# Performance work log

Hardware: AMD Instinct MI355X
Metric: run time of the kernel (lower is better)

The kernel has to match this reference:

```python
import jax, jax.numpy as jnp
import numpy as np

N_NODES = 100000
N_EDGES = 3200000
N_GRAPHS = 1024
K = 32  # total number of kernels (num_kernel1..4 = 8 each)


def setup_inputs() -> dict:
    key = jax.random.key(0)
    ks = jax.random.split(key, 20)
    inp = {
        'x': jax.random.normal(ks[0], (N_NODES, 5), jnp.float32),
        'p': jax.random.normal(ks[1], (N_NODES, 3), jnp.float32),
        'edge_attr': jax.random.normal(ks[2], (N_EDGES, 1), jnp.float32),
        'Wx0': jax.random.normal(ks[3], (5, K), jnp.float32) * 0.3,
        'Wx1': jax.random.normal(ks[4], (K, K), jnp.float32) * 0.1,
        'Wx2': jax.random.normal(ks[5], (K, K), jnp.float32) * 0.1,
        'Wp0': jax.random.normal(ks[6], (3, K), jnp.float32) * 0.3,
        'Wp1': jax.random.normal(ks[7], (3, K), jnp.float32) * 0.3,
        'Wp2': jax.random.normal(ks[8], (3, K), jnp.float32) * 0.3,
        'We0': jax.random.normal(ks[9], (1, K), jnp.float32) * 0.3,
        'We1': jax.random.normal(ks[10], (1, K), jnp.float32) * 0.3,
        'We2': jax.random.normal(ks[11], (1, K), jnp.float32) * 0.3,
        'b0': jax.random.normal(ks[12], (K,), jnp.float32) * 0.1,
        'b1': jax.random.normal(ks[13], (K,), jnp.float32) * 0.1,
        'b2': jax.random.normal(ks[14], (K,), jnp.float32) * 0.1,
        'Wh': jax.random.normal(ks[15], (K, 1), jnp.float32) * 0.1,
        'bh': jax.random.normal(ks[16], (1,), jnp.float32) * 0.1,
        'edge_index': jax.random.randint(ks[17], (2, N_EDGES), 0, N_NODES, jnp.int64 if jax.config.jax_enable_x64 else jnp.int32),
        'batch': jnp.sort(jax.random.randint(ks[18], (N_NODES,), 0, N_GRAPHS, jnp.int64 if jax.config.jax_enable_x64 else jnp.int32)),
    }
    return inp


def _gnn_forward(x, p, edge_attr, Wxs, Wps, Wes, bs, edge_index):
    src, dst = edge_index[0], edge_index[1]
    p_rel = p[src] - p[dst]                      # [E, 3] relative positions
    h = x
    for Wx, Wp, We, b in zip(Wxs, Wps, Wes, bs):
        # kernel similarity per edge: gather neighbor feats + geometry, score vs K kernels
        msg = jnp.tanh(h[src] @ Wx + p_rel @ Wp + edge_attr @ We + b)   # [E, K]
        sim_sc = jax.ops.segment_sum(msg, dst, num_segments=N_NODES)    # [N, K] node sim scores
        # MolGCN.propagate: message(sim_sc_j) with aggr='add'
        h = jax.ops.segment_sum(sim_sc[src], dst, num_segments=N_NODES)  # [N, K]
    return h


def reference(x, p, edge_attr, Wx0, Wx1, Wx2, Wp0, Wp1, Wp2, We0, We1, We2,
              b0, b1, b2, Wh, bh, edge_index, batch):
    h = _gnn_forward(x, p, edge_attr, (Wx0, Wx1, Wx2), (Wp0, Wp1, Wp2),
                     (We0, We1, We2), (b0, b1, b2), edge_index)
    # global_mean_pool over graphs
    sums = jax.ops.segment_sum(h, batch, num_segments=N_GRAPHS)          # [G, K]
    cnt = jax.ops.segment_sum(jnp.ones((N_NODES,), h.dtype), batch, num_segments=N_GRAPHS)
    graph_rep = sums / jnp.maximum(cnt, 1.0)[:, None]                    # [G, K]
    pred = graph_rep @ Wh + bh                                           # [G, 1]
    return (pred, graph_rep)
```

## Files before the change

### kernel.cpp

```cpp
#include <hip/hip_runtime.h>
#include <hip/hip_fp16.h>

#define K_DIM 32
#define BN 256
#define MAXBUCK 512
#define CAP 10240
#define TANH_SCALE 2.8853900817779268f

typedef float f32x2 __attribute__((ext_vector_type(2)));

__device__ __forceinline__ void pk_add(f32x2& acc, f32x2 v) {
    asm("v_pk_add_f32 %0, %1, %0" : "+v"(acc) : "v"(v));
}


__global__ void k_bcnt(const int* __restrict__ dst, int* __restrict__ bcnt,
                       int E, int nbuck) {
    __shared__ int h[MAXBUCK];
    for (int i = threadIdx.x; i < nbuck; i += blockDim.x) h[i] = 0;
    __syncthreads();
    for (int e = blockIdx.x * blockDim.x + threadIdx.x; e < E; e += gridDim.x * blockDim.x)
        atomicAdd(&h[dst[e] >> 8], 1);
    __syncthreads();
    for (int i = threadIdx.x; i < nbuck; i += blockDim.x)
        if (h[i]) atomicAdd(&bcnt[i], h[i]);
}

__global__ void k_bscan(const int* __restrict__ bcnt, int* __restrict__ boff,
                        int* __restrict__ gcur, int nbuck, int total) {
    __shared__ int sm[256];
    __shared__ int carry;
    int t = threadIdx.x;
    if (t == 0) carry = 0;
    __syncthreads();
    for (int base = 0; base < nbuck; base += 256) {
        int v = (base + t < nbuck) ? bcnt[base + t] : 0;
        sm[t] = v;
        __syncthreads();
        #pragma unroll
        for (int d = 1; d < 256; d <<= 1) {
            int tv = (t >= d) ? sm[t - d] : 0;
            __syncthreads();
            sm[t] += tv;
            __syncthreads();
        }
        int excl = carry + sm[t] - v;
        if (base + t < nbuck) { boff[base + t] = excl; gcur[base + t] = excl; }
        __syncthreads();
        if (t == 0) carry += sm[255];
        __syncthreads();
    }
    if (t == 0) boff[nbuck] = total;
}

__global__ void k_bscatter(const int* __restrict__ src, const int* __restrict__ dst,
                           const float* __restrict__ ea, int* __restrict__ gcur,
                           uint2* __restrict__ rec, int E, int nbuck) {
    __shared__ int lcnt[MAXBUCK];
    __shared__ int lbase[MAXBUCK];
    const int nb = gridDim.x;
    const long c0 = (long)E * blockIdx.x / nb;
    const long c1 = (long)E * (blockIdx.x + 1) / nb;
    for (int i = threadIdx.x; i < nbuck; i += blockDim.x) lcnt[i] = 0;
    __syncthreads();
    for (long e = c0 + threadIdx.x; e < c1; e += blockDim.x)
        atomicAdd(&lcnt[dst[e] >> 8], 1);
    __syncthreads();
    for (int i = threadIdx.x; i < nbuck; i += blockDim.x) {
        int c = lcnt[i];
        lbase[i] = c ? atomicAdd(&gcur[i], c) : 0;
    }
    __syncthreads();
    for (int i = threadIdx.x; i < nbuck; i += blockDim.x) lcnt[i] = 0;
    __syncthreads();
    for (long e = c0 + threadIdx.x; e < c1; e += blockDim.x) {
        int d = dst[e];
        int b = d >> 8;
        int rank = atomicAdd(&lcnt[b], 1);
        unsigned meta = ((unsigned)(d & 255) << 17) | (unsigned)src[e];
        rec[lbase[b] + rank] = make_uint2(meta, __float_as_uint(ea[e]));
    }
}

__global__ void k_blocal(const uint2* __restrict__ rec, uint2* __restrict__ rec2,
                         int* __restrict__ srcs2, const int* __restrict__ boff,
                         int* __restrict__ off, int N, int E) {
    __shared__ uint2 sB[CAP];
    __shared__ int cnt[BN];
    __shared__ int base[BN];
    __shared__ int sm[BN];
    const int b = blockIdx.x;
    const int tid = threadIdx.x;
    int e0 = boff[b], e1 = boff[b + 1];
    int tot = e1 - e0;
    cnt[tid] = 0;
    __syncthreads();
    for (int i = tid; i < tot; i += 256)
        atomicAdd(&cnt[rec[e0 + i].x >> 17], 1);
    __syncthreads();
    int v = cnt[tid];
    sm[tid] = v;
    __syncthreads();
    #pragma unroll
    for (int d = 1; d < 256; d <<= 1) {
        int tv = (tid >= d) ? sm[tid - d] : 0;
        __syncthreads();
        sm[tid] += tv;
        __syncthreads();
    }
    base[tid] = sm[tid] - v;
    int n = b * BN + tid;
    if (n < N) off[n] = e0 + base[tid];
    if (b == 0 && tid == 0) off[N] = E;
    cnt[tid] = 0;
    __syncthreads();
    for (int i = tid; i < tot; i += 256) {
        uint2 r = rec[e0 + i];
        int dl = r.x >> 17;
        int rank = atomicAdd(&cnt[dl], 1);
        unsigned s = r.x & 0x1FFFFu;
        float eaf = __uint_as_float(r.y);
        unsigned hb = (unsigned)__half_as_ushort(__float2half(eaf));
        sB[base[dl] + rank] = make_uint2(s, (hb << 16) | hb);
    }
    __syncthreads();
    for (int i = tid; i < tot; i += 256) {
        uint2 r = sB[i];
        rec2[e0 + i] = r;
        srcs2[e0 + i] = (int)r.x;
    }
}

__global__ void k_initdummy(__half* __restrict__ Mh, __half* __restrict__ simh, int N) {
    int i = threadIdx.x;
    Mh[N * 32 + i] = __ushort_as_half((unsigned short)0x7C00);
    simh[N * 32 + i] = __ushort_as_half((unsigned short)0);
}


__global__ void k_node_gemm5(const float* __restrict__ h, const float* __restrict__ p,
                             const float* __restrict__ Wx, const float* __restrict__ Wp,
                             __half* __restrict__ Mh, int n_nodes) {
    __shared__ float sWx[5 * 32];
    __shared__ float sWp[96];
    for (int i = threadIdx.x; i < 5 * 32; i += blockDim.x) sWx[i] = Wx[i] * TANH_SCALE;
    if (threadIdx.x < 96) sWp[threadIdx.x] = Wp[threadIdx.x] * TANH_SCALE;
    __syncthreads();
    const int k = threadIdx.x & 31;
    int n = blockIdx.x * (blockDim.x >> 5) + (threadIdx.x >> 5);
    if (n >= n_nodes) return;
    float hv = (k < 5) ? h[n * 5 + k] : 0.0f;
    float pv = (k < 3) ? p[n * 3 + k] : 0.0f;
    float acc = 0.0f;
    #pragma unroll
    for (int j = 0; j < 5; ++j) acc = fmaf(__shfl(hv, j, 32), sWx[j * 32 + k], acc);
    #pragma unroll
    for (int j = 0; j < 3; ++j) acc = fmaf(__shfl(pv, j, 32), sWp[j * 32 + k], acc);
    Mh[n * 32 + k] = __float2half(acc);
}

__global__ void k_edge_msg(const __half* __restrict__ Mh, const float* __restrict__ p,
                           const int* __restrict__ off, const uint2* __restrict__ rec,
                           const float* __restrict__ Wp, const float* __restrict__ We,
                           const float* __restrict__ bias,
                           __half* __restrict__ simh, int N) {
    __shared__ uint2 stage[8][32];
    const int l = threadIdx.x & 31;
    const int c = l & 15;
    const int q = l >> 4;
    const int grp = threadIdx.x >> 5;
    int n = blockIdx.x * 8 + grp;
    if (n >= N) return;

    const __half2* Mh2 = (const __half2*)Mh;

    float2 wef = ((const float2*)We)[c];
    __half2 we2 = __floats2half2_rn(wef.x * TANH_SCALE, wef.y * TANH_SCALE);
    float2 b2  = ((const float2*)bias)[c];
    float2 wp0 = ((const float2*)Wp)[c];
    float2 wp1 = ((const float2*)(Wp + 32))[c];
    float2 wp2 = ((const float2*)(Wp + 64))[c];
    float pn = (l < 3) ? p[n * 3 + l] : 0.0f;
    float pn0 = __shfl(pn, 0, 32), pn1 = __shfl(pn, 1, 32), pn2 = __shfl(pn, 2, 32);
    __half2 cnst2 = __floats2half2_rn(
        (b2.x - (pn0 * wp0.x + pn1 * wp1.x + pn2 * wp2.x)) * TANH_SCALE,
        (b2.y - (pn0 * wp0.y + pn1 * wp1.y + pn2 * wp2.y)) * TANH_SCALE);
    const __half2 one2  = __floats2half2_rn(1.0f, 1.0f);
    const __half2 zero2 = __floats2half2_rn(0.0f, 0.0f);

    float fx = 0.0f, fy = 0.0f;
    int e0 = off[n], e1 = off[n + 1];
    for (int base = e0; base < e1; base += 32) {
        int m = min(32, e1 - base);
        uint2 r = (l < m) ? rec[base + l] : make_uint2((unsigned)N, 0u);
        stage[grp][l] = r;
        __half2 acc2 = zero2;
        for (int j = 0; j < m; j += 16) {
            __half2 mv[8], av[8];
            #pragma unroll
            for (int u = 0; u < 8; ++u) {
                uint2 e = stage[grp][j + 2 * u + q];
                unsigned eb = e.y;
                av[u] = *(const __half2*)&eb;
                mv[u] = Mh2[e.x * 16 + c];
            }
            #pragma unroll
            for (int u = 0; u < 8; ++u) {
                __half2 arg = __hadd2(__hfma2(av[u], we2, cnst2), mv[u]);
                __half2 ex  = h2exp2(arg);
                __half2 rr  = h2rcp(__hadd2(ex, one2));
                acc2 = __hadd2(acc2, rr);
            }
        }
        fx += __low2float(acc2);
        fy += __high2float(acc2);
    }
    fx += __shfl_xor(fx, 16, 32);
    fy += __shfl_xor(fy, 16, 32);
    float deg = (float)(e1 - e0);
    if (l < 16)
        ((__half2*)simh)[n * 16 + c] =
            __floats2half2_rn(fmaf(-2.0f, fx, deg), fmaf(-2.0f, fy, deg));
}

template <int FUSE>
__global__ void k_prop_gemm(const __half* __restrict__ simh, const int* __restrict__ off,
                            const int* __restrict__ srcs, const float* __restrict__ p,
                            const float* __restrict__ Wx, const float* __restrict__ Wp,
                            __half* __restrict__ outMh, float* __restrict__ outF,
                            int N) {
    __shared__ float sWx[1024];
    __shared__ int stageS[8][32];
    if (FUSE) {
        for (int i = threadIdx.x; i < 1024; i += blockDim.x) sWx[i] = Wx[i] * TANH_SCALE;
        __syncthreads();
    }
    const int l = threadIdx.x & 31;
    const int c = l & 15;
    const int q = l >> 4;
    const int grp = threadIdx.x >> 5;
    int n = blockIdx.x * 8 + grp;
    if (n >= N) return;

    const __half2* sim2 = (const __half2*)simh;
    f32x2 facc = {0.0f, 0.0f};
    int e0 = off[n], e1 = off[n + 1];
    for (int base = e0; base < e1; base += 32) {
        int m = min(32, e1 - base);
        stageS[grp][l] = (l < m) ? srcs[base + l] : N;
        for (int j = 0; j < m; j += 16) {
            __half2 v[8];
            #pragma unroll
            for (int u = 0; u < 8; ++u) {
                int s = stageS[grp][j + 2 * u + q];
                v[u] = sim2[s * 16 + c];
            }
            #pragma unroll
            for (int u = 0; u < 8; ++u) {
                float2 fv = __half22float2(v[u]);
                f32x2 t = {fv.x, fv.y};
                pk_add(facc, t);
            }
        }
    }
    float fx = facc.x, fy = facc.y;
    fx += __shfl_xor(fx, 16, 32);
    fy += __shfl_xor(fy, 16, 32);

    if (!FUSE) {
        if (l < 16) ((float2*)outF)[n * 16 + c] = make_float2(fx, fy);
        return;
    }
    float mm = 0.0f;
    #pragma unroll
    for (int i = 0; i < 16; ++i) {
        float hx = __shfl(fx, i, 32);
        float hy = __shfl(fy, i, 32);
        mm = fmaf(hx, sWx[(2 * i) * 32 + l], mm);
        mm = fmaf(hy, sWx[(2 * i + 1) * 32 + l], mm);
    }
    float pv = (l < 3) ? p[n * 3 + l] : 0.0f;
    float pp = __shfl(pv, 0, 32) * Wp[l] + __shfl(pv, 1, 32) * Wp[32 + l]
             + __shfl(pv, 2, 32) * Wp[64 + l];
    mm = fmaf(pp, TANH_SCALE, mm);
    outMh[n * 32 + l] = __float2half(mm);
}


__global__ void k_pool(const float* __restrict__ h, const int* __restrict__ batch,
                       const float* __restrict__ Wh, const float* __restrict__ bh,
                       float* __restrict__ out, int n_nodes, int n_graphs) {
    __shared__ int sLo, sHi;
    __shared__ float red[256];
    int g = blockIdx.x;
    if (threadIdx.x == 0) {
        int lo = 0, hi = n_nodes;
        while (lo < hi) { int m = (lo + hi) >> 1; if (batch[m] < g) lo = m + 1; else hi = m; }
        sLo = lo;
        lo = 0; hi = n_nodes; int g1 = g + 1;
        while (lo < hi) { int m = (lo + hi) >> 1; if (batch[m] < g1) lo = m + 1; else hi = m; }
        sHi = lo;
    }
    __syncthreads();
    int lo = sLo, hi = sHi;
    int k = threadIdx.x & 31, r = threadIdx.x >> 5;
    float acc = 0.0f;
    for (int n = lo + r; n < hi; n += 8) acc += h[n * 32 + k];
    red[threadIdx.x] = acc;
    __syncthreads();
    if (threadIdx.x < 32) {
        float s = 0.0f;
        #pragma unroll
        for (int r2 = 0; r2 < 8; ++r2) s += red[r2 * 32 + k];
        float c = (float)(hi - lo);
        float rep = s / fmaxf(c, 1.0f);
        out[n_graphs + g * 32 + k] = rep;
        float t = rep * Wh[k];
        #pragma unroll
        for (int d = 16; d > 0; d >>= 1) t += __shfl_down(t, d, 32);
        if (k == 0) out[g] = t + bh[0];
    }
}


extern "C" void kernel_launch(void* const* d_in, const int* in_sizes, int n_in,
                              void* d_out, int out_size, void* d_ws, size_t ws_size,
                              hipStream_t stream) {
    const float* x   = (const float*)d_in[0];
    const float* p   = (const float*)d_in[1];
    const float* ea  = (const float*)d_in[2];
    const float* Wx0 = (const float*)d_in[3];
    const float* Wx1 = (const float*)d_in[4];
    const float* Wx2 = (const float*)d_in[5];
    const float* Wp0 = (const float*)d_in[6];
    const float* Wp1 = (const float*)d_in[7];
    const float* Wp2 = (const float*)d_in[8];
    const float* We0 = (const float*)d_in[9];
    const float* We1 = (const float*)d_in[10];
    const float* We2 = (const float*)d_in[11];
    const float* b0  = (const float*)d_in[12];
    const float* b1  = (const float*)d_in[13];
    const float* b2  = (const float*)d_in[14];
    const float* Wh  = (const float*)d_in[15];
    const float* bh  = (const float*)d_in[16];
    const int* edge_index = (const int*)d_in[17];
    const int* batch      = (const int*)d_in[18];

    const int N = in_sizes[0] / 5;
    const int E = in_sizes[17] / 2;
    const int G = out_size / 33;
    const int nbuck = (N + BN - 1) / BN;

    const int* srcp = edge_index;
    const int* dstp = edge_index + E;

    char* w = (char*)d_ws;
    auto alloc = [&](size_t bytes) -> void* {
        void* r = (void*)w;
        w += (bytes + 255) & ~(size_t)255;
        return r;
    };
    int*    bcnt  = (int*)alloc((size_t)nbuck * 4);
    int*    boff  = (int*)alloc((size_t)(nbuck + 1) * 4);
    int*    gcur  = (int*)alloc((size_t)nbuck * 4);
    int*    off   = (int*)alloc((size_t)(N + 1) * 4);
    uint2*  rec   = (uint2*)alloc((size_t)E * 8);
    uint2*  rec2  = (uint2*)alloc((size_t)E * 8);
    int*    srcs2 = (int*)alloc((size_t)E * 4);
    __half* Mh    = (__half*)alloc((size_t)(N + 1) * K_DIM * 2);
    __half* simh  = (__half*)alloc((size_t)(N + 1) * K_DIM * 2);
    float*  hB    = (float*)alloc((size_t)N * K_DIM * 4);

    (void)hipMemsetAsync(bcnt, 0, (size_t)nbuck * 4, stream);
    k_bcnt<<<1024, 256, 0, stream>>>(dstp, bcnt, E, nbuck);
    k_bscan<<<1, 256, 0, stream>>>(bcnt, boff, gcur, nbuck, E);
    k_bscatter<<<256, 1024, 0, stream>>>(srcp, dstp, ea, gcur, rec, E, nbuck);
    k_blocal<<<nbuck, 256, 0, stream>>>(rec, rec2, srcs2, boff, off, N, E);
    k_initdummy<<<1, 32, 0, stream>>>(Mh, simh, N);

    const int NB = (N + 7) / 8;

    k_node_gemm5<<<NB, 256, 0, stream>>>(x, p, Wx0, Wp0, Mh, N);
    k_edge_msg<<<NB, 256, 0, stream>>>(Mh, p, off, rec2, Wp0, We0, b0, simh, N);
    k_prop_gemm<1><<<NB, 256, 0, stream>>>(simh, off, srcs2, p, Wx1, Wp1, Mh, nullptr, N);
    k_edge_msg<<<NB, 256, 0, stream>>>(Mh, p, off, rec2, Wp1, We1, b1, simh, N);
    k_prop_gemm<1><<<NB, 256, 0, stream>>>(simh, off, srcs2, p, Wx2, Wp2, Mh, nullptr, N);
    k_edge_msg<<<NB, 256, 0, stream>>>(Mh, p, off, rec2, Wp2, We2, b2, simh, N);
    k_prop_gemm<0><<<NB, 256, 0, stream>>>(simh, off, srcs2, p, nullptr, nullptr, nullptr, hB, N);

    k_pool<<<G, 256, 0, stream>>>(hB, batch, Wh, bh, (float*)d_out, N, G);
}
```

Before: 398.3 us.

## Split 32-wide features into two 16-column halves for cache-resident gathers

Node features and similarity scores are stored as two separate 16-column half arrays, and the edge-message and propagation kernels run twice per layer, once per half. Each half-array is about 3.2MB, so the random gathers can stay cache-resident instead of hitting the full 6.4MB table. The node GEMM is moved out of the propagation kernel into a separate 32x32 kernel reading fp32 hF. Edge record and source index loads now use nontemporal hints. The cost is reading the edge lists twice per layer and adding extra kernel launches.

Result: slower. 576.7 us (+44.8%).

```diff
diff --git a/kernel.cpp b/kernel.cpp
--- a/kernel.cpp
+++ b/kernel.cpp
@@ -1,7 +1,6 @@
 #include <hip/hip_runtime.h>
 #include <hip/hip_fp16.h>
 
-#define K_DIM 32
 #define BN 256
 #define MAXBUCK 512
 #define CAP 10240
@@ -131,16 +130,22 @@
     }
 }
 
-__global__ void k_initdummy(__half* __restrict__ Mh, __half* __restrict__ simh, int N) {
+__global__ void k_initdummy(__half* __restrict__ Mh0, __half* __restrict__ Mh1,
+                            __half* __restrict__ s0, __half* __restrict__ s1, int N) {
     int i = threadIdx.x;
-    Mh[N * 32 + i] = __ushort_as_half((unsigned short)0x7C00);
-    simh[N * 32 + i] = __ushort_as_half((unsigned short)0);
+    if (i < 16) {
+        Mh0[N * 16 + i] = __ushort_as_half((unsigned short)0x7C00);
+        Mh1[N * 16 + i] = __ushort_as_half((unsigned short)0x7C00);
+        s0[N * 16 + i] = __ushort_as_half((unsigned short)0);
+        s1[N * 16 + i] = __ushort_as_half((unsigned short)0);
+    }
 }
 
 
 __global__ void k_node_gemm5(const float* __restrict__ h, const float* __restrict__ p,
                              const float* __restrict__ Wx, const float* __restrict__ Wp,
-                             __half* __restrict__ Mh, int n_nodes) {
+                             __half* __restrict__ Mh0, __half* __restrict__ Mh1,
+                             int n_nodes) {
     __shared__ float sWx[5 * 32];
     __shared__ float sWp[96];
     for (int i = threadIdx.x; i < 5 * 32; i += blockDim.x) sWx[i] = Wx[i] * TANH_SCALE;
@@ -156,30 +161,54 @@
     for (int j = 0; j < 5; ++j) acc = fmaf(__shfl(hv, j, 32), sWx[j * 32 + k], acc);
     #pragma unroll
     for (int j = 0; j < 3; ++j) acc = fmaf(__shfl(pv, j, 32), sWp[j * 32 + k], acc);
-    Mh[n * 32 + k] = __float2half(acc);
-}
-
-__global__ void k_edge_msg(const __half* __restrict__ Mh, const float* __restrict__ p,
-                           const int* __restrict__ off, const uint2* __restrict__ rec,
-                           const float* __restrict__ Wp, const float* __restrict__ We,
-                           const float* __restrict__ bias,
-                           __half* __restrict__ simh, int N) {
+    __half hh = __float2half(acc);
+    if (k < 16) Mh0[n * 16 + k] = hh; else Mh1[n * 16 + (k & 15)] = hh;
+}
+
+__global__ void k_node_gemm32(const float* __restrict__ hF, const float* __restrict__ p,
+                              const float* __restrict__ Wx, const float* __restrict__ Wp,
+                              __half* __restrict__ Mh0, __half* __restrict__ Mh1,
+                              int n_nodes) {
+    __shared__ float sWx[1024];
+    __shared__ float sWp[96];
+    for (int i = threadIdx.x; i < 1024; i += blockDim.x) sWx[i] = Wx[i] * TANH_SCALE;
+    if (threadIdx.x < 96) sWp[threadIdx.x] = Wp[threadIdx.x] * TANH_SCALE;
+    __syncthreads();
+    const int k = threadIdx.x & 31;
+    int n = blockIdx.x * (blockDim.x >> 5) + (threadIdx.x >> 5);
+    if (n >= n_nodes) return;
+    float hv = hF[n * 32 + k];
+    float pv = (k < 3) ? p[n * 3 + k] : 0.0f;
+    float acc = 0.0f;
+    #pragma unroll
+    for (int j = 0; j < 32; ++j) acc = fmaf(__shfl(hv, j, 32), sWx[j * 32 + k], acc);
+    #pragma unroll
+    for (int j = 0; j < 3; ++j) acc = fmaf(__shfl(pv, j, 32), sWp[j * 32 + k], acc);
+    __half hh = __float2half(acc);
+    if (k < 16) Mh0[n * 16 + k] = hh; else Mh1[n * 16 + (k & 15)] = hh;
+}
+
+__global__ void k_edge_half(const __half* __restrict__ MhH, const float* __restrict__ p,
+                            const int* __restrict__ off, const uint2* __restrict__ rec,
+                            const float* __restrict__ WpH, const float* __restrict__ WeH,
+                            const float* __restrict__ biasH,
+                            __half* __restrict__ simH, int N) {
     __shared__ uint2 stage[8][32];
     const int l = threadIdx.x & 31;
-    const int c = l & 15;
-    const int q = l >> 4;
+    const int c = l & 7;
+    const int q = l >> 3;
     const int grp = threadIdx.x >> 5;
     int n = blockIdx.x * 8 + grp;
     if (n >= N) return;
 
-    const __half2* Mh2 = (const __half2*)Mh;
-
-    float2 wef = ((const float2*)We)[c];
+    const __half2* MhH2 = (const __half2*)MhH;
+
+    float2 wef = ((const float2*)WeH)[c];
     __half2 we2 = __floats2half2_rn(wef.x * TANH_SCALE, wef.y * TANH_SCALE);
-    float2 b2  = ((const float2*)bias)[c];
-    float2 wp0 = ((const float2*)Wp)[c];
-    float2 wp1 = ((const float2*)(Wp + 32))[c];
-    float2 wp2 = ((const float2*)(Wp + 64))[c];
+    float2 b2  = ((const float2*)biasH)[c];
+    float2 wp0 = ((const float2*)WpH)[c];
+    float2 wp1 = ((const float2*)(WpH + 32))[c];
+    float2 wp2 = ((const float2*)(WpH + 64))[c];
     float pn = (l < 3) ? p[n * 3 + l] : 0.0f;
     float pn0 = __shfl(pn, 0, 32), pn1 = __shfl(pn, 1, 32), pn2 = __shfl(pn, 2, 32);
     __half2 cnst2 = __floats2half2_rn(
@@ -188,102 +217,74 @@
     const __half2 one2  = __floats2half2_rn(1.0f, 1.0f);
     const __half2 zero2 = __floats2half2_rn(0.0f, 0.0f);
 
+    const unsigned long long* rec8 = (const unsigned long long*)rec;
     float fx = 0.0f, fy = 0.0f;
     int e0 = off[n], e1 = off[n + 1];
     for (int base = e0; base < e1; base += 32) {
         int m = min(32, e1 - base);
-        uint2 r = (l < m) ? rec[base + l] : make_uint2((unsigned)N, 0u);
-        stage[grp][l] = r;
+        unsigned long long rv = (l < m) ? __builtin_nontemporal_load(rec8 + base + l)
+                                        : (unsigned long long)(unsigned)N;
+        stage[grp][l] = make_uint2((unsigned)rv, (unsigned)(rv >> 32));
+        __half2 mv[8], av[8];
+        #pragma unroll
+        for (int u = 0; u < 8; ++u) {
+            uint2 e = stage[grp][4 * u + q];
+            unsigned eb = e.y;
+            av[u] = *(const __half2*)&eb;
+            mv[u] = MhH2[e.x * 8 + c];
+        }
         __half2 acc2 = zero2;
-        for (int j = 0; j < m; j += 16) {
-            __half2 mv[8], av[8];
-            #pragma unroll
-            for (int u = 0; u < 8; ++u) {
-                uint2 e = stage[grp][j + 2 * u + q];
-                unsigned eb = e.y;
-                av[u] = *(const __half2*)&eb;
-                mv[u] = Mh2[e.x * 16 + c];
-            }
-            #pragma unroll
-            for (int u = 0; u < 8; ++u) {
-                __half2 arg = __hadd2(__hfma2(av[u], we2, cnst2), mv[u]);
-                __half2 ex  = h2exp2(arg);
-                __half2 rr  = h2rcp(__hadd2(ex, one2));
-                acc2 = __hadd2(acc2, rr);
-            }
+        #pragma unroll
+        for (int u = 0; u < 8; ++u) {
+            __half2 arg = __hadd2(__hfma2(av[u], we2, cnst2), mv[u]);
+            acc2 = __hadd2(acc2, h2rcp(__hadd2(h2exp2(arg), one2)));
         }
         fx += __low2float(acc2);
         fy += __high2float(acc2);
     }
-    fx += __shfl_xor(fx, 16, 32);
-    fy += __shfl_xor(fy, 16, 32);
+    fx += __shfl_xor(fx, 8, 32); fx += __shfl_xor(fx, 16, 32);
+    fy += __shfl_xor(fy, 8, 32); fy += __shfl_xor(fy, 16, 32);
     float deg = (float)(e1 - e0);
-    if (l < 16)
-        ((__half2*)simh)[n * 16 + c] =
+    if (l < 8)
+        ((__half2*)simH)[n * 8 + c] =
             __floats2half2_rn(fmaf(-2.0f, fx, deg), fmaf(-2.0f, fy, deg));
 }
 
-template <int FUSE>
-__global__ void k_prop_gemm(const __half* __restrict__ simh, const int* __restrict__ off,
-                            const int* __restrict__ srcs, const float* __restrict__ p,
-                            const float* __restrict__ Wx, const float* __restrict__ Wp,
-                            __half* __restrict__ outMh, float* __restrict__ outF,
-                            int N) {
-    __shared__ float sWx[1024];
+__global__ void k_prop_half(const __half* __restrict__ simH, const int* __restrict__ off,
+                            const int* __restrict__ srcs, float* __restrict__ hF,
+                            int colbase, int N) {
     __shared__ int stageS[8][32];
-    if (FUSE) {
-        for (int i = threadIdx.x; i < 1024; i += blockDim.x) sWx[i] = Wx[i] * TANH_SCALE;
-        __syncthreads();
-    }
     const int l = threadIdx.x & 31;
-    const int c = l & 15;
-    const int q = l >> 4;
+    const int c = l & 7;
+    const int q = l >> 3;
     const int grp = threadIdx.x >> 5;
     int n = blockIdx.x * 8 + grp;
     if (n >= N) return;
 
-    const __half2* sim2 = (const __half2*)simh;
+    const __half2* sim2 = (const __half2*)simH;
     f32x2 facc = {0.0f, 0.0f};
     int e0 = off[n], e1 = off[n + 1];
     for (int base = e0; base < e1; base += 32) {
         int m = min(32, e1 - base);
-        stageS[grp][l] = (l < m) ? srcs[base + l] : N;
-        for (int j = 0; j < m; j += 16) {
-            __half2 v[8];
-            #pragma unroll
-            for (int u = 0; u < 8; ++u) {
-                int s = stageS[grp][j + 2 * u + q];
-                v[u] = sim2[s * 16 + c];
-            }
-            #pragma unroll
-            for (int u = 0; u < 8; ++u) {
-                float2 fv = __half22float2(v[u]);
-                f32x2 t = {fv.x, fv.y};
-                pk_add(facc, t);
-            }
+        stageS[grp][l] = (l < m) ? __builtin_nontemporal_load(srcs + base + l) : N;
+        __half2 v[8];
+        #pragma unroll
+        for (int u = 0; u < 8; ++u) {
+            int s = stageS[grp][4 * u + q];
+            v[u] = sim2[s * 8 + c];
         }
+        #pragma unroll
+        for (int u = 0; u < 8; ++u) {
+            float2 fv = __half22float2(v[u]);
+            f32x2 t = {fv.x, fv.y};
+            pk_add(facc, t);
+        }
     }
     float fx = facc.x, fy = facc.y;
-    fx += __shfl_xor(fx, 16, 32);
-    fy += __shfl_xor(fy, 16, 32);
-
-    if (!FUSE) {
-        if (l < 16) ((float2*)outF)[n * 16 + c] = make_float2(fx, fy);
-        return;
-    }
-    float mm = 0.0f;
-    #pragma unroll
-    for (int i = 0; i < 16; ++i) {
-        float hx = __shfl(fx, i, 32);
-        float hy = __shfl(fy, i, 32);
-        mm = fmaf(hx, sWx[(2 * i) * 32 + l], mm);
-        mm = fmaf(hy, sWx[(2 * i + 1) * 32 + l], mm);
-    }
-    float pv = (l < 3) ? p[n * 3 + l] : 0.0f;
-    float pp = __shfl(pv, 0, 32) * Wp[l] + __shfl(pv, 1, 32) * Wp[32 + l]
-             + __shfl(pv, 2, 32) * Wp[64 + l];
-    mm = fmaf(pp, TANH_SCALE, mm);
-    outMh[n * 32 + l] = __float2half(mm);
+    fx += __shfl_xor(fx, 8, 32); fx += __shfl_xor(fx, 16, 32);
+    fy += __shfl_xor(fy, 8, 32); fy += __shfl_xor(fy, 16, 32);
+    if (l < 8)
+        ((float2*)(hF + n * 32 + colbase))[c] = make_float2(fx, fy);
 }
 
 
@@ -367,26 +368,36 @@
     uint2*  rec   = (uint2*)alloc((size_t)E * 8);
     uint2*  rec2  = (uint2*)alloc((size_t)E * 8);
     int*    srcs2 = (int*)alloc((size_t)E * 4);
-    __half* Mh    = (__half*)alloc((size_t)(N + 1) * K_DIM * 2);
-    __half* simh  = (__half*)alloc((size_t)(N + 1) * K_DIM * 2);
-    float*  hB    = (float*)alloc((size_t)N * K_DIM * 4);
+    __half* Mh0   = (__half*)alloc((size_t)(N + 1) * 16 * 2);
+    __half* Mh1   = (__half*)alloc((size_t)(N + 1) * 16 * 2);
+    __half* sim0  = (__half*)alloc((size_t)(N + 1) * 16 * 2);
+    __half* sim1  = (__half*)alloc((size_t)(N + 1) * 16 * 2);
+    float*  hF    = (float*)alloc((size_t)N * 32 * 4);
 
     (void)hipMemsetAsync(bcnt, 0, (size_t)nbuck * 4, stream);
     k_bcnt<<<1024, 256, 0, stream>>>(dstp, bcnt, E, nbuck);
     k_bscan<<<1, 256, 0, stream>>>(bcnt, boff, gcur, nbuck, E);
     k_bscatter<<<256, 1024, 0, stream>>>(srcp, dstp, ea, gcur, rec, E, nbuck);
     k_blocal<<<nbuck, 256, 0, stream>>>(rec, rec2, srcs2, boff, off, N, E);
-    k_initdummy<<<1, 32, 0, stream>>>(Mh, simh, N);
+    k_initdummy<<<1, 64, 0, stream>>>(Mh0, Mh1, sim0, sim1, N);
 
     const int NB = (N + 7) / 8;
 
-    k_node_gemm5<<<NB, 256, 0, stream>>>(x, p, Wx0, Wp0, Mh, N);
-    k_edge_msg<<<NB, 256, 0, stream>>>(Mh, p, off, rec2, Wp0, We0, b0, simh, N);
-    k_prop_gemm<1><<<NB, 256, 0, stream>>>(simh, off, srcs2, p, Wx1, Wp1, Mh, nullptr, N);
-    k_edge_msg<<<NB, 256, 0, stream>>>(Mh, p, off, rec2, Wp1, We1, b1, simh, N);
-    k_prop_gemm<1><<<NB, 256, 0, stream>>>(simh, off, srcs2, p, Wx2, Wp2, Mh, nullptr, N);
-    k_edge_msg<<<NB, 256, 0, stream>>>(Mh, p, off, rec2, Wp2, We2, b2, simh, N);
-    k_prop_gemm<0><<<NB, 256, 0, stream>>>(simh, off, srcs2, p, nullptr, nullptr, nullptr, hB, N);
-
-    k_pool<<<G, 256, 0, stream>>>(hB, batch, Wh, bh, (float*)d_out, N, G);
-}
+    k_node_gemm5<<<NB, 256, 0, stream>>>(x, p, Wx0, Wp0, Mh0, Mh1, N);
+    k_edge_half<<<NB, 256, 0, stream>>>(Mh0, p, off, rec2, Wp0, We0, b0, sim0, N);
+    k_edge_half<<<NB, 256, 0, stream>>>(Mh1, p, off, rec2, Wp0 + 16, We0 + 16, b0 + 16, sim1, N);
+    k_prop_half<<<NB, 256, 0, stream>>>(sim0, off, srcs2, hF, 0, N);
+    k_prop_half<<<NB, 256, 0, stream>>>(sim1, off, srcs2, hF, 16, N);
+    k_node_gemm32<<<NB, 256, 0, stream>>>(hF, p, Wx1, Wp1, Mh0, Mh1, N);
+    k_edge_half<<<NB, 256, 0, stream>>>(Mh0, p, off, rec2, Wp1, We1, b1, sim0, N);
+    k_edge_half<<<NB, 256, 0, stream>>>(Mh1, p, off, rec2, Wp1 + 16, We1 + 16, b1 + 16, sim1, N);
+    k_prop_half<<<NB, 256, 0, stream>>>(sim0, off, srcs2, hF, 0, N);
+    k_prop_half<<<NB, 256, 0, stream>>>(sim1, off, srcs2, hF, 16, N);
+    k_node_gemm32<<<NB, 256, 0, stream>>>(hF, p, Wx2, Wp2, Mh0, Mh1, N);
+    k_edge_half<<<NB, 256, 0, stream>>>(Mh0, p, off, rec2, Wp2, We2, b2, sim0, N);
+    k_edge_half<<<NB, 256, 0, stream>>>(Mh1, p, off, rec2, Wp2 + 16, We2 + 16, b2 + 16, sim1, N);
+    k_prop_half<<<NB, 256, 0, stream>>>(sim0, off, srcs2, hF, 0, N);
+    k_prop_half<<<NB, 256, 0, stream>>>(sim1, off, srcs2, hF, 16, N);
+
+    k_pool<<<G, 256, 0, stream>>>(hF, batch, Wh, bh, (float*)d_out, N, G);
+}
```
